# Optimization experiments

Hardware: AMD Instinct MI355X
Metric: run time of the kernel (lower is better)

The kernel has to match this reference:

```python
import jax, jax.numpy as jnp
import numpy as np

G = 8          # n_games
D_IN = 512     # per-game input dim (equal for all games)
H1 = 1024
H2 = 1024
A = 128        # max_actions
B = 8192       # batch rows


def setup_inputs() -> dict:
    key = jax.random.key(0)
    ks = jax.random.split(key, 9)
    state = jax.random.normal(ks[0], (B, D_IN), dtype=jnp.float32)
    idx = jax.random.randint(ks[1], (B,), 0, G, dtype=jnp.int32)
    # per-game input linears: uniform(-1/sqrt(fan_in), 1/sqrt(fan_in))
    lim1 = 1.0 / np.sqrt(D_IN)
    W1 = jax.random.uniform(ks[2], (G, D_IN, H1), minval=-lim1, maxval=lim1, dtype=jnp.float32)
    b1 = jax.random.uniform(ks[3], (G, H1), minval=-lim1, maxval=lim1, dtype=jnp.float32)
    # shared linear
    lim2 = 1.0 / np.sqrt(H1)
    W2 = jax.random.uniform(ks[4], (H1, H2), minval=-lim2, maxval=lim2, dtype=jnp.float32)
    b2 = jax.random.uniform(ks[5], (H2,), minval=-lim2, maxval=lim2, dtype=jnp.float32)
    # per-game output heads: uniform(-0.003, 0.003)
    W3 = jax.random.uniform(ks[6], (G, H2, A), minval=-0.003, maxval=0.003, dtype=jnp.float32)
    b3 = jax.random.uniform(ks[7], (G, A), minval=-0.003, maxval=0.003, dtype=jnp.float32)
    return {"state": state, "idx": idx, "W1": W1, "b1": b1, "W2": W2, "b2": b2, "W3": W3, "b3": b3}


def reference(state, idx, W1, b1, W2, b2, W3, b3):
    # Torch code concatenates per-game groups in sorted-unique-idx order,
    # i.e. a stable permutation of rows by idx; reproduce exactly.
    perm = jnp.argsort(idx, stable=True)          # [B]
    s = state[perm]                               # [B, D_IN]
    g = idx[perm]                                 # [B] game of each permuted row
    # routed first layer: compute all games then gather per-row game
    h1_all = jnp.einsum('bd,gdh->bgh', s, W1) + b1            # [B, G, H1]
    h1 = jax.nn.relu(jnp.take_along_axis(h1_all, g[:, None, None], axis=1)[:, 0, :])  # [B, H1]
    h_f = jax.nn.relu(h1 @ W2 + b2)                            # [B, H2]
    a = jnp.tanh(jnp.einsum('bh,gha->bga', h_f, W3) + b3)      # [B, G, A]
    # NOTE: original gathers heads with the ORIGINAL (unpermuted) idx,
    # even though rows of `a` are in permuted order. Reproduce faithfully.
    out = jnp.take_along_axis(a, idx[:, None, None], axis=1)[:, 0, :]  # [B, A]
    return out
```

## Files before the change

### kernel.cpp

```cpp
#include <hip/hip_runtime.h>
#include <math.h>

#define G_GAMES 8
#define D_IN 512
#define H1 1024
#define H2 1024
#define A_DIM 128
#define B_ROWS 8192

typedef short bf16x8 __attribute__((ext_vector_type(8)));
typedef float f32x4 __attribute__((ext_vector_type(4)));

#define WS_OFF   0u
#define WS_PERM  256u
#define WS_SPERM 33280u
#define WS_W1T   (WS_SPERM + B_ROWS*D_IN*2u)
#define WS_W2T   (WS_W1T + G_GAMES*D_IN*H1*2u)
#define WS_W3T   (WS_W2T + (unsigned)H1*H2*2u)
#define WS_H1    (WS_W3T + G_GAMES*H2*A_DIM*2u)
#define WS_HF    WS_SPERM

__device__ __forceinline__ unsigned short f2bf(float x) {
  union { float f; unsigned int u; } v; v.f = x;
  unsigned int r = v.u + 0x7fffu + ((v.u >> 16) & 1u);
  return (unsigned short)(r >> 16);
}

__device__ __forceinline__ unsigned int cvt_pk_bf16(float lo, float hi) {
  unsigned int r;
  asm("v_cvt_pk_bf16_f32 %0, %1, %2" : "=v"(r) : "v"(lo), "v"(hi));
  return r;
}

__device__ __forceinline__ void async_load16(const void* gptr, void* ldsptr) {
  __builtin_amdgcn_global_load_lds(
      (const __attribute__((address_space(1))) unsigned int*)gptr,
      (__attribute__((address_space(3))) unsigned int*)ldsptr,
      16, 0, 0);
}

__device__ void sort_256(const int* __restrict__ idx, int* __restrict__ perm,
                         int* __restrict__ off) {
  __shared__ int wtot[4][9];
  __shared__ int wbase[4][9];
  __shared__ int offs[9];
  const int t = threadIdx.x, lane = t & 63, wave = t >> 6;
  int my[32];
#pragma unroll
  for (int i = 0; i < 8; ++i) {
    const int4 a = *(const int4*)(idx + t * 32 + i * 4);
    my[i*4+0] = a.x; my[i*4+1] = a.y; my[i*4+2] = a.z; my[i*4+3] = a.w;
  }
  int local[8];
#pragma unroll
  for (int g = 0; g < 8; ++g) {
    int c = 0;
#pragma unroll
    for (int i = 0; i < 32; ++i) c += (my[i] == g) ? 1 : 0;
    local[g] = c;
  }
  int incl[8];
#pragma unroll
  for (int g = 0; g < 8; ++g) {
    int v = local[g];
#pragma unroll
    for (int d = 1; d < 64; d <<= 1) {
      const int n = __shfl_up(v, d);
      if (lane >= d) v += n;
    }
    incl[g] = v;
  }
  if (lane == 63) {
#pragma unroll
    for (int g = 0; g < 8; ++g) wtot[wave][g] = incl[g];
  }
  __syncthreads();
  if (t < 8) {
    int s = 0;
#pragma unroll
    for (int w = 0; w < 4; ++w) { wbase[w][t] = s; s += wtot[w][t]; }
    wtot[0][t] = s;
  }
  __syncthreads();
  if (t == 0) {
    int s = 0;
#pragma unroll
    for (int g = 0; g < 8; ++g) { offs[g] = s; off[g] = s; s += wtot[0][g]; }
    offs[8] = s; off[8] = s;
  }
  __syncthreads();
#pragma unroll
  for (int g = 0; g < 8; ++g) {
    int sg = offs[g] + wbase[wave][g] + (incl[g] - local[g]);
#pragma unroll
    for (int i = 0; i < 32; ++i) {
      const bool m = (my[i] == g);
      if (m) perm[sg] = t * 32 + i;
      sg += m ? 1 : 0;
    }
  }
}

__device__ void trans_tile_ws(char* ldsbuf, const float* __restrict__ in,
                              unsigned short* __restrict__ out,
                              int R, int C, int xt, int yt, int z) {
  in  += (size_t)z * R * C;
  out += (size_t)z * R * C;
  unsigned short (*tl)[68] = (unsigned short(*)[68])ldsbuf;
  const int c0 = xt * 64, r0 = yt * 64;
  const int t = threadIdx.x;
#pragma unroll
  for (int pass = 0; pass < 4; ++pass) {
    const int id = pass * 256 + t;
    const int r = id >> 4, f4c = (id & 15) << 2;
    const float4 v = *(const float4*)(in + (size_t)(r0 + r) * C + c0 + f4c);
    uint2 w;
    w.x = cvt_pk_bf16(v.x, v.y);
    w.y = cvt_pk_bf16(v.z, v.w);
    *(uint2*)&tl[r][f4c] = w;
  }
  __syncthreads();
#pragma unroll
  for (int pass = 0; pass < 2; ++pass) {
    const int cc = t >> 2, k0 = ((t & 3) << 3) + (pass << 5);
    unsigned short u[8];
#pragma unroll
    for (int j = 0; j < 8; ++j) u[j] = tl[k0 + j][cc];
    uint4 v;
    v.x = (unsigned)u[0] | ((unsigned)u[1] << 16);
    v.y = (unsigned)u[2] | ((unsigned)u[3] << 16);
    v.z = (unsigned)u[4] | ((unsigned)u[5] << 16);
    v.w = (unsigned)u[6] | ((unsigned)u[7] << 16);
    *(uint4*)(out + (size_t)(c0 + cc) * R + r0 + k0) = v;
  }
}

__device__ __forceinline__ bool seg_map(const int* __restrict__ off, int T,
                                        int& g, int& seg1, int& row0) {
  int base = 0;
  for (int gg = 0; gg < 8; ++gg) {
    const int s = off[gg], e = off[gg + 1];
    const int nt = (e - s + 127) >> 7;
    if (T < base + nt) { g = gg; seg1 = e; row0 = s + (T - base) * 128; return true; }
    base += nt;
  }
  return false;
}

__device__ __forceinline__ bool seg_map16(const int* __restrict__ off, int T,
                                          int& g, int& seg1, int& row0) {
  int base = 0;
  for (int gg = 0; gg < 8; ++gg) {
    const int s = off[gg], e = off[gg + 1];
    const int nt = (e - s + 15) >> 4;
    if (T < base + nt) { g = gg; seg1 = e; row0 = s + (T - base) * 16; return true; }
    base += nt;
  }
  return false;
}

__device__ __forceinline__ void epilogue_bf16(char* smem, const f32x4 acc[4][4],
                                              const float* bj, int tid,
                                              unsigned short* __restrict__ outp,
                                              size_t ldOut, int row0, int col0,
                                              int vrows) {
  const int lane = tid & 63, wave = tid >> 6;
  const int wm = wave & 1, wn = wave >> 1;
  const int sw = lane & 15, quad = lane >> 4;
  __syncthreads();
#pragma unroll
  for (int i = 0; i < 4; ++i)
#pragma unroll
    for (int j = 0; j < 4; ++j)
#pragma unroll
      for (int r = 0; r < 4; ++r) {
        const int row = wm * 64 + i * 16 + quad * 4 + r;
        const int col = wn * 64 + j * 16 + sw;
        const float v = fmaxf(acc[i][j][r] + bj[j], 0.0f);
        *(unsigned short*)(smem + row * 264 + col * 2) = f2bf(v);
      }
  __syncthreads();
#pragma unroll
  for (int q = 0; q < 8; ++q) {
    const int idxq = q * 256 + tid;
    const int row = idxq >> 4, ch = idxq & 15;
    if (row < vrows) {
      const uint2 lo = *(const uint2*)(smem + row * 264 + ch * 16);
      const uint2 hi = *(const uint2*)(smem + row * 264 + ch * 16 + 8);
      uint4 v; v.x = lo.x; v.y = lo.y; v.z = hi.x; v.w = hi.y;
      *(uint4*)((char*)outp + ((size_t)(row0 + row) * ldOut + col0 + ch * 8) * 2) = v;
    }
  }
}

__device__ void gemm1_tile(const float* __restrict__ state,
                           const int* __restrict__ perm,
                           const unsigned short* __restrict__ W1T,
                           const float* __restrict__ b1,
                           const int* __restrict__ off,
                           unsigned short* __restrict__ h1out,
                           int T, char* smem, int tid) {
  int g, seg1, row0;
  if (!seg_map(off, T % 72, g, seg1, row0)) return;
  const int col0 = (T / 72) * 128;
  const int lane = tid & 63, wave = tid >> 6;
  const int wm = wave & 1, wn = wave >> 1;
  const int sw = lane & 15, quad = lane >> 4;
  const int lc = lane & 7;
  const int gcol = ((lane & 7) ^ (lane >> 3)) << 3;
  const float* aS[4];
  int ldsA[4];
  const unsigned short* bP[4];
#pragma unroll
  for (int c = 0; c < 4; ++c) {
    const int rl = wave * 32 + c * 8 + (lane >> 3);
    int p = row0 + rl;
    if (p > seg1 - 1) p = seg1 - 1;
    aS[c]  = state + (size_t)perm[p] * D_IN + lc * 8;
    ldsA[c] = rl * 128 + ((lc ^ (rl & 7)) << 4);
    bP[c]  = W1T + (size_t)g * H1 * D_IN + (size_t)(col0 + rl) * D_IN + gcol;
  }
  char* A0 = smem;          char* A1 = smem + 16384;
  char* B0 = smem + 32768;  char* B1 = smem + 49152;
  const int mA = wm * 64 + sw, nB = wn * 64 + sw;
  f32x4 acc[4][4] = {};
  {
    float4 t0[4], t1[4];
#pragma unroll
    for (int c = 0; c < 4; ++c) {
      t0[c] = *(const float4*)(aS[c]);
      t1[c] = *(const float4*)(aS[c] + 4);
      async_load16(bP[c], B0 + (wave * 32 + c * 8) * 128);
    }
#pragma unroll
    for (int c = 0; c < 4; ++c) {
      uint4 pk;
      pk.x = cvt_pk_bf16(t0[c].x, t0[c].y);
      pk.y = cvt_pk_bf16(t0[c].z, t0[c].w);
      pk.z = cvt_pk_bf16(t1[c].x, t1[c].y);
      pk.w = cvt_pk_bf16(t1[c].z, t1[c].w);
      *(uint4*)(A0 + ldsA[c]) = pk;
    }
  }
  const int NIT = D_IN >> 6;
#pragma unroll 2
  for (int k = 0; k < NIT; ++k) {
    __syncthreads();
    char* A = (k & 1) ? A1 : A0;
    char* B = (k & 1) ? B1 : B0;
    float4 t0[4], t1[4];
    const bool pf = (k + 1 < NIT);
    if (pf) {
      char* Bn = (k & 1) ? B0 : B1;
      const int koff = (k + 1) << 6;
#pragma unroll
      for (int c = 0; c < 4; ++c) {
        t0[c] = *(const float4*)(aS[c] + koff);
        t1[c] = *(const float4*)(aS[c] + koff + 4);
        async_load16(bP[c] + koff, Bn + (wave * 32 + c * 8) * 128);
      }
    }
#pragma unroll
    for (int ks = 0; ks < 2; ++ks) {
      const int u = ((((ks << 2) + quad) ^ (sw & 7)) << 4);
      bf16x8 aF[4], bF[4];
#pragma unroll
      for (int i = 0; i < 4; ++i) {
        aF[i] = *(const bf16x8*)(A + (mA + i * 16) * 128 + u);
        bF[i] = *(const bf16x8*)(B + (nB + i * 16) * 128 + u);
      }
#pragma unroll
      for (int i = 0; i < 4; ++i)
#pragma unroll
        for (int j = 0; j < 4; ++j)
          acc[i][j] = __builtin_amdgcn_mfma_f32_16x16x32_bf16(aF[i], bF[j], acc[i][j], 0, 0, 0);
    }
    if (pf) {
      char* An = (k & 1) ? A0 : A1;
#pragma unroll
      for (int c = 0; c < 4; ++c) {
        uint4 pk;
        pk.x = cvt_pk_bf16(t0[c].x, t0[c].y);
        pk.y = cvt_pk_bf16(t0[c].z, t0[c].w);
        pk.z = cvt_pk_bf16(t1[c].x, t1[c].y);
        pk.w = cvt_pk_bf16(t1[c].z, t1[c].w);
        *(uint4*)(An + ldsA[c]) = pk;
      }
    }
  }
  const float* bg = b1 + g * H1;
  float bj[4];
#pragma unroll
  for (int j = 0; j < 4; ++j) bj[j] = bg[col0 + wn * 64 + j * 16 + sw];
  const int vrows = min(128, seg1 - row0);
  epilogue_bf16(smem, acc, bj, tid, h1out, H1, row0, col0, vrows);
}

__device__ void gemm2_tile(const unsigned short* __restrict__ h1in,
                           const unsigned short* __restrict__ W2T,
                           const float* __restrict__ b2,
                           unsigned short* __restrict__ hfout,
                           int T, char* smem, int tid) {
  const int row0 = (T & 63) * 128, col0 = (T >> 6) * 128;
  const int lane = tid & 63, wave = tid >> 6;
  const int wm = wave & 1, wn = wave >> 1;
  const int sw = lane & 15, quad = lane >> 4;
  const int gcol = ((lane & 7) ^ (lane >> 3)) << 3;
  const unsigned short* aP[4];
  const unsigned short* bP[4];
#pragma unroll
  for (int c = 0; c < 4; ++c) {
    const int rl = wave * 32 + c * 8 + (lane >> 3);
    aP[c] = h1in + (size_t)(row0 + rl) * H1 + gcol;
    bP[c] = W2T + (size_t)(col0 + rl) * H1 + gcol;
  }
  char* A0 = smem;          char* A1 = smem + 16384;
  char* B0 = smem + 32768;  char* B1 = smem + 49152;
  const int mA = wm * 64 + sw, nB = wn * 64 + sw;
  f32x4 acc[4][4] = {};
#pragma unroll
  for (int c = 0; c < 4; ++c) {
    async_load16(aP[c], A0 + (wave * 32 + c * 8) * 128);
    async_load16(bP[c], B0 + (wave * 32 + c * 8) * 128);
  }
  const int NIT = H1 >> 6;
#pragma unroll 2
  for (int k = 0; k < NIT; ++k) {
    __syncthreads();
    char* A = (k & 1) ? A1 : A0;
    char* B = (k & 1) ? B1 : B0;
    if (k + 1 < NIT) {
      char* An = (k & 1) ? A0 : A1;
      char* Bn = (k & 1) ? B0 : B1;
      const int koff = (k + 1) << 6;
#pragma unroll
      for (int c = 0; c < 4; ++c) {
        async_load16(aP[c] + koff, An + (wave * 32 + c * 8) * 128);
        async_load16(bP[c] + koff, Bn + (wave * 32 + c * 8) * 128);
      }
    }
#pragma unroll
    for (int ks = 0; ks < 2; ++ks) {
      const int u = ((((ks << 2) + quad) ^ (sw & 7)) << 4);
      bf16x8 aF[4], bF[4];
#pragma unroll
      for (int i = 0; i < 4; ++i) {
        aF[i] = *(const bf16x8*)(A + (mA + i * 16) * 128 + u);
        bF[i] = *(const bf16x8*)(B + (nB + i * 16) * 128 + u);
      }
#pragma unroll
      for (int i = 0; i < 4; ++i)
#pragma unroll
        for (int j = 0; j < 4; ++j)
          acc[i][j] = __builtin_amdgcn_mfma_f32_16x16x32_bf16(aF[i], bF[j], acc[i][j], 0, 0, 0);
    }
  }
  float bj[4];
#pragma unroll
  for (int j = 0; j < 4; ++j) bj[j] = b2[col0 + wn * 64 + j * 16 + sw];
  epilogue_bf16(smem, acc, bj, tid, hfout, H2, row0, col0, 128);
}

__device__ void gemm3_tile(const unsigned short* __restrict__ hf,
                           const unsigned short* __restrict__ W3T,
                           const float* __restrict__ b3,
                           const int* __restrict__ off,
                           const int* __restrict__ perm,
                           float* __restrict__ outp,
                           int T, char* smem, int tid) {
  int g, seg1, row0;
  if (!seg_map16(off, T, g, seg1, row0)) return;
  const int lane = tid & 63, wave = tid >> 6;
  const int sw = lane & 15, quad = lane >> 4;
  const int gcol = ((lane & 7) ^ (lane >> 3)) << 3;
  int q0 = row0 + (wave & 1) * 8 + (lane >> 3);
  if (q0 > seg1 - 1) q0 = seg1 - 1;
  const unsigned short* aP = hf + (size_t)perm[q0] * H2 + gcol;
  const unsigned short* bP[4];
#pragma unroll
  for (int c = 0; c < 4; ++c) {
    const int rl = wave * 32 + c * 8 + (lane >> 3);
    bP[c] = W3T + (size_t)g * A_DIM * H2 + (size_t)rl * H2 + gcol;
  }
  char* A0 = smem;         char* A1 = smem + 4096;
  char* B0 = smem + 8192;  char* B1 = smem + 24576;
  const int nB = wave * 32 + sw;
  f32x4 acc[2] = {};
  if (wave < 2) async_load16(aP, A0 + (wave * 8) * 128);
#pragma unroll
  for (int c = 0; c < 4; ++c)
    async_load16(bP[c], B0 + (wave * 32 + c * 8) * 128);
#pragma unroll 2
  for (int k = 0; k < (H2 >> 6); ++k) {
    __syncthreads();
    char* A = (k & 1) ? A1 : A0;
    char* B = (k & 1) ? B1 : B0;
    if (k + 1 < (H2 >> 6)) {
      char* An = (k & 1) ? A0 : A1;
      char* Bn = (k & 1) ? B0 : B1;
      const int koff = (k + 1) << 6;
      if (wave < 2) async_load16(aP + koff, An + (wave * 8) * 128);
#pragma unroll
      for (int c = 0; c < 4; ++c)
        async_load16(bP[c] + koff, Bn + (wave * 32 + c * 8) * 128);
    }
#pragma unroll
    for (int ks = 0; ks < 2; ++ks) {
      const int u = ((((ks << 2) + quad) ^ (sw & 7)) << 4);
      const bf16x8 aF = *(const bf16x8*)(A + sw * 128 + u);
      bf16x8 bF[2];
#pragma unroll
      for (int j = 0; j < 2; ++j)
        bF[j] = *(const bf16x8*)(B + (nB + j * 16) * 128 + u);
#pragma unroll
      for (int j = 0; j < 2; ++j)
        acc[j] = __builtin_amdgcn_mfma_f32_16x16x32_bf16(aF, bF[j], acc[j], 0, 0, 0);
    }
  }
  const float* bg = b3 + g * A_DIM;
  float bj[2];
#pragma unroll
  for (int j = 0; j < 2; ++j) bj[j] = bg[wave * 32 + j * 16 + sw];
  __syncthreads();
#pragma unroll
  for (int j = 0; j < 2; ++j)
#pragma unroll
    for (int r = 0; r < 4; ++r) {
      const int row = quad * 4 + r;
      const int col = wave * 32 + j * 16 + sw;
      *(float*)(smem + row * 528 + col * 4) = tanhf(acc[j][r] + bj[j]);
    }
  __syncthreads();
#pragma unroll
  for (int qq = 0; qq < 2; ++qq) {
    const int idxq = qq * 256 + tid;
    const int row = idxq >> 5, ch = idxq & 31;
    if (row0 + row < seg1) {
      const uint4 v = *(const uint4*)(smem + row * 528 + ch * 16);
      *(uint4*)((char*)outp + ((size_t)perm[row0 + row] * A_DIM + ch * 4) * 4) = v;
    }
  }
}

__global__ __launch_bounds__(256) void k_pre(const float* __restrict__ W1,
                                             const int* __restrict__ idx,
                                             unsigned short* __restrict__ W1T,
                                             int* __restrict__ perm,
                                             int* __restrict__ off) {
  __shared__ __align__(16) char tsmem[8704];
  const int b = blockIdx.x;
  if (b == 0) {
    sort_256(idx, perm, off);
  } else {
    const int r0 = b - 1, z = r0 >> 7, r = r0 & 127;
    trans_tile_ws(tsmem, W1, W1T, D_IN, H1, r & 15, r >> 4, z);
  }
}

__global__ __launch_bounds__(256, 2) void k_g1(const float* __restrict__ state,
                                               const int* __restrict__ perm,
                                               const unsigned short* __restrict__ W1T,
                                               const float* __restrict__ b1,
                                               const int* __restrict__ off,
                                               const float* __restrict__ W2,
                                               const float* __restrict__ W3,
                                               unsigned short* __restrict__ W2T,
                                               unsigned short* __restrict__ W3T,
                                               unsigned short* __restrict__ h1out) {
  __shared__ __align__(16) char smem[65536];
  const int b = blockIdx.x;
  if (b >= 576) {
    const int t = b - 576;
    if (t < 256) {
      trans_tile_ws(smem, W2, W2T, H1, H2, t & 15, t >> 4, 0);
    } else {
      const int r = (t - 256) & 31, z = (t - 256) >> 5;
      trans_tile_ws(smem, W3, W3T, H2, A_DIM, r & 1, r >> 1, z);
    }
    return;
  }
  gemm1_tile(state, perm, W1T, b1, off, h1out, b, smem, threadIdx.x);
}

__global__ __launch_bounds__(256) void k_g2(const unsigned short* __restrict__ h1in,
                                            const unsigned short* __restrict__ W2T,
                                            const float* __restrict__ b2,
                                            unsigned short* __restrict__ hfout) {
  __shared__ __align__(16) char smem[65536];
  gemm2_tile(h1in, W2T, b2, hfout, blockIdx.x, smem, threadIdx.x);
}

__global__ __launch_bounds__(256) void k_g3(const unsigned short* __restrict__ hf,
                                            const unsigned short* __restrict__ W3T,
                                            const float* __restrict__ b3,
                                            const int* __restrict__ off,
                                            const int* __restrict__ perm,
                                            float* __restrict__ outp) {
  __shared__ __align__(16) char smem[40960];
  gemm3_tile(hf, W3T, b3, off, perm, outp, blockIdx.x, smem, threadIdx.x);
}

extern "C" void kernel_launch(void* const* d_in, const int* in_sizes, int n_in,
                              void* d_out, int out_size, void* d_ws, size_t ws_size,
                              hipStream_t stream) {
  (void)in_sizes; (void)n_in; (void)out_size; (void)ws_size;
  const float* state = (const float*)d_in[0];
  const int*   idx   = (const int*)d_in[1];
  const float* W1    = (const float*)d_in[2];
  const float* b1    = (const float*)d_in[3];
  const float* W2    = (const float*)d_in[4];
  const float* b2    = (const float*)d_in[5];
  const float* W3    = (const float*)d_in[6];
  const float* b3    = (const float*)d_in[7];
  float* outp = (float*)d_out;
  char* ws = (char*)d_ws;
  int* off  = (int*)(ws + WS_OFF);
  int* perm = (int*)(ws + WS_PERM);
  unsigned short* W1T   = (unsigned short*)(ws + WS_W1T);
  unsigned short* W2T   = (unsigned short*)(ws + WS_W2T);
  unsigned short* W3T   = (unsigned short*)(ws + WS_W3T);
  unsigned short* h1    = (unsigned short*)(ws + WS_H1);
  unsigned short* hf    = (unsigned short*)(ws + WS_HF);

  hipLaunchKernelGGL(k_pre, dim3(1025), dim3(256), 0, stream,
                     W1, idx, W1T, perm, off);
  hipLaunchKernelGGL(k_g1, dim3(1088), dim3(256), 0, stream,
                     state, perm, W1T, b1, off, W2, W3, W2T, W3T, h1);
  hipLaunchKernelGGL(k_g2, dim3(512), dim3(256), 0, stream, h1, W2T, b2, hf);
  hipLaunchKernelGGL(k_g3, dim3(520), dim3(256), 0, stream, hf, W3T, b3, off, perm, outp);
}
```

Measured before the change: 157.3 us.

## Parallelize stable sort across 32 blocks and move W2/W3 transposes earlier

Replaces the single-block 8192-element counting sort with a two-phase parallel version: 32 blocks build per-chunk histograms alongside the W1 transpose, then a new kernel scatters ranks computed with ballot/popcount. The W2/W3 transposes move out of the GEMM1 kernel into the new sort kernel, so GEMM1 launches only its own tiles. This removes the serial single-block sort that sat on the critical path of the first kernel. The cost is one extra kernel launch and a global histogram buffer placed in the h1 workspace region.

Measured after the change: 152.7 us. -2.9%, faster.

```diff
diff --git a/kernel.cpp b/kernel.cpp
--- a/kernel.cpp
+++ b/kernel.cpp
@@ -19,6 +19,7 @@
 #define WS_W3T   (WS_W2T + (unsigned)H1*H2*2u)
 #define WS_H1    (WS_W3T + G_GAMES*H2*A_DIM*2u)
 #define WS_HF    WS_SPERM
+#define WS_CNT   WS_H1
 
 __device__ __forceinline__ unsigned short f2bf(float x) {
   union { float f; unsigned int u; } v; v.f = x;
@@ -39,66 +40,65 @@
       16, 0, 0);
 }
 
-__device__ void sort_256(const int* __restrict__ idx, int* __restrict__ perm,
-                         int* __restrict__ off) {
-  __shared__ int wtot[4][9];
-  __shared__ int wbase[4][9];
-  __shared__ int offs[9];
+__device__ void hist_chunk(const int* __restrict__ idx, int* __restrict__ cnt,
+                           int chunk) {
+  __shared__ int wc[4][8];
   const int t = threadIdx.x, lane = t & 63, wave = t >> 6;
-  int my[32];
-#pragma unroll
-  for (int i = 0; i < 8; ++i) {
-    const int4 a = *(const int4*)(idx + t * 32 + i * 4);
-    my[i*4+0] = a.x; my[i*4+1] = a.y; my[i*4+2] = a.z; my[i*4+3] = a.w;
-  }
-  int local[8];
-#pragma unroll
-  for (int g = 0; g < 8; ++g) {
-    int c = 0;
-#pragma unroll
-    for (int i = 0; i < 32; ++i) c += (my[i] == g) ? 1 : 0;
-    local[g] = c;
-  }
-  int incl[8];
-#pragma unroll
-  for (int g = 0; g < 8; ++g) {
-    int v = local[g];
-#pragma unroll
-    for (int d = 1; d < 64; d <<= 1) {
-      const int n = __shfl_up(v, d);
-      if (lane >= d) v += n;
-    }
-    incl[g] = v;
-  }
-  if (lane == 63) {
-#pragma unroll
-    for (int g = 0; g < 8; ++g) wtot[wave][g] = incl[g];
-  }
+  const int g = idx[chunk * 256 + t];
+#pragma unroll
+  for (int g0 = 0; g0 < 8; ++g0) {
+    const unsigned long long m = __ballot(g == g0);
+    if (lane == 0) wc[wave][g0] = __popcll(m);
+  }
+  __syncthreads();
+  if (t < 8) cnt[chunk * 8 + t] = wc[0][t] + wc[1][t] + wc[2][t] + wc[3][t];
+}
+
+__device__ void scatter_chunk(const int* __restrict__ idx,
+                              const int* __restrict__ cnt,
+                              int* __restrict__ perm, int* __restrict__ off,
+                              int chunk) {
+  __shared__ int scnt[256];
+  __shared__ int cbase[8];
+  __shared__ int wcn[4][8];
+  const int t = threadIdx.x, lane = t & 63, wave = t >> 6;
+  scnt[t] = cnt[t];
+  const int g = idx[chunk * 256 + t];
   __syncthreads();
   if (t < 8) {
-    int s = 0;
-#pragma unroll
-    for (int w = 0; w < 4; ++w) { wbase[w][t] = s; s += wtot[w][t]; }
-    wtot[0][t] = s;
-  }
-  __syncthreads();
-  if (t == 0) {
-    int s = 0;
-#pragma unroll
-    for (int g = 0; g < 8; ++g) { offs[g] = s; off[g] = s; s += wtot[0][g]; }
-    offs[8] = s; off[8] = s;
-  }
-  __syncthreads();
-#pragma unroll
-  for (int g = 0; g < 8; ++g) {
-    int sg = offs[g] + wbase[wave][g] + (incl[g] - local[g]);
-#pragma unroll
-    for (int i = 0; i < 32; ++i) {
-      const bool m = (my[i] == g);
-      if (m) perm[sg] = t * 32 + i;
-      sg += m ? 1 : 0;
-    }
-  }
+    int gt[8];
+#pragma unroll
+    for (int gg = 0; gg < 8; ++gg) {
+      int s = 0;
+      for (int c = 0; c < 32; ++c) s += scnt[c * 8 + gg];
+      gt[gg] = s;
+    }
+    int go = 0;
+#pragma unroll
+    for (int gg = 0; gg < 8; ++gg) if (gg < t) go += gt[gg];
+    int cp = 0;
+    for (int c = 0; c < chunk; ++c) cp += scnt[c * 8 + t];
+    cbase[t] = go + cp;
+    if (chunk == 0) {
+      off[t] = go;
+      if (t == 7) off[8] = go + gt[7];
+    }
+  }
+  const unsigned long long below = (1ull << lane) - 1ull;
+  int rank = 0;
+#pragma unroll
+  for (int g0 = 0; g0 < 8; ++g0) {
+    const unsigned long long m = __ballot(g == g0);
+    const int r = __popcll(m & below);
+    if (g0 == g) rank = r;
+    if (lane == 0) wcn[wave][g0] = __popcll(m);
+  }
+  __syncthreads();
+  int wof = 0;
+#pragma unroll
+  for (int w = 0; w < 4; ++w)
+    if (w < wave) wof += wcn[w][g];
+  perm[cbase[g] + wof + rank] = chunk * 256 + t;
 }
 
 __device__ void trans_tile_ws(char* ldsbuf, const float* __restrict__ in,
@@ -445,15 +445,35 @@
 __global__ __launch_bounds__(256) void k_pre(const float* __restrict__ W1,
                                              const int* __restrict__ idx,
                                              unsigned short* __restrict__ W1T,
-                                             int* __restrict__ perm,
-                                             int* __restrict__ off) {
+                                             int* __restrict__ cnt) {
   __shared__ __align__(16) char tsmem[8704];
   const int b = blockIdx.x;
-  if (b == 0) {
-    sort_256(idx, perm, off);
+  if (b < 32) {
+    hist_chunk(idx, cnt, b);
   } else {
-    const int r0 = b - 1, z = r0 >> 7, r = r0 & 127;
+    const int r0 = b - 32, z = r0 >> 7, r = r0 & 127;
     trans_tile_ws(tsmem, W1, W1T, D_IN, H1, r & 15, r >> 4, z);
+  }
+}
+
+__global__ __launch_bounds__(256) void k_sort(const int* __restrict__ idx,
+                                              const int* __restrict__ cnt,
+                                              const float* __restrict__ W2,
+                                              const float* __restrict__ W3,
+                                              int* __restrict__ perm,
+                                              int* __restrict__ off,
+                                              unsigned short* __restrict__ W2T,
+                                              unsigned short* __restrict__ W3T) {
+  __shared__ __align__(16) char tsmem[8704];
+  const int b = blockIdx.x;
+  if (b < 32) {
+    scatter_chunk(idx, cnt, perm, off, b);
+  } else if (b < 288) {
+    const int t = b - 32;
+    trans_tile_ws(tsmem, W2, W2T, H1, H2, t & 15, t >> 4, 0);
+  } else {
+    const int t = b - 288, r = t & 31, z = t >> 5;
+    trans_tile_ws(tsmem, W3, W3T, H2, A_DIM, r & 1, r >> 1, z);
   }
 }
 
@@ -462,24 +482,9 @@
                                                const unsigned short* __restrict__ W1T,
                                                const float* __restrict__ b1,
                                                const int* __restrict__ off,
-                                               const float* __restrict__ W2,
-                                               const float* __restrict__ W3,
-                                               unsigned short* __restrict__ W2T,
-                                               unsigned short* __restrict__ W3T,
                                                unsigned short* __restrict__ h1out) {
   __shared__ __align__(16) char smem[65536];
-  const int b = blockIdx.x;
-  if (b >= 576) {
-    const int t = b - 576;
-    if (t < 256) {
-      trans_tile_ws(smem, W2, W2T, H1, H2, t & 15, t >> 4, 0);
-    } else {
-      const int r = (t - 256) & 31, z = (t - 256) >> 5;
-      trans_tile_ws(smem, W3, W3T, H2, A_DIM, r & 1, r >> 1, z);
-    }
-    return;
-  }
-  gemm1_tile(state, perm, W1T, b1, off, h1out, b, smem, threadIdx.x);
+  gemm1_tile(state, perm, W1T, b1, off, h1out, blockIdx.x, smem, threadIdx.x);
 }
 
 __global__ __launch_bounds__(256) void k_g2(const unsigned short* __restrict__ h1in,
@@ -516,16 +521,18 @@
   char* ws = (char*)d_ws;
   int* off  = (int*)(ws + WS_OFF);
   int* perm = (int*)(ws + WS_PERM);
+  int* cnt  = (int*)(ws + WS_CNT);
   unsigned short* W1T   = (unsigned short*)(ws + WS_W1T);
   unsigned short* W2T   = (unsigned short*)(ws + WS_W2T);
   unsigned short* W3T   = (unsigned short*)(ws + WS_W3T);
   unsigned short* h1    = (unsigned short*)(ws + WS_H1);
   unsigned short* hf    = (unsigned short*)(ws + WS_HF);
 
-  hipLaunchKernelGGL(k_pre, dim3(1025), dim3(256), 0, stream,
-                     W1, idx, W1T, perm, off);
-  hipLaunchKernelGGL(k_g1, dim3(1088), dim3(256), 0, stream,
-                     state, perm, W1T, b1, off, W2, W3, W2T, W3T, h1);
+  hipLaunchKernelGGL(k_pre, dim3(1056), dim3(256), 0, stream, W1, idx, W1T, cnt);
+  hipLaunchKernelGGL(k_sort, dim3(544), dim3(256), 0, stream,
+                     idx, cnt, W2, W3, perm, off, W2T, W3T);
+  hipLaunchKernelGGL(k_g1, dim3(576), dim3(256), 0, stream,
+                     state, perm, W1T, b1, off, h1);
   hipLaunchKernelGGL(k_g2, dim3(512), dim3(256), 0, stream, h1, W2T, b2, hf);
   hipLaunchKernelGGL(k_g3, dim3(520), dim3(256), 0, stream, hf, W3T, b3, off, perm, outp);
 }
```
